# Performance work log

Measured on AMD Instinct MI355X. Metric: run time of the kernel, lower is better.

## Reference

```python
import jax, jax.numpy as jnp
import numpy as np

N_NODES = 100000
N_EDGES = 1250000
D_IN = 32
H = 64
EPS = 1e-5


def layer_norm(x, g, b):
    mu = jnp.mean(x, axis=-1, keepdims=True)
    var = jnp.mean(jnp.square(x - mu), axis=-1, keepdims=True)
    return (x - mu) * jax.lax.rsqrt(var + EPS) * g + b


def setup_inputs() -> dict:
    key = jax.random.key(0)
    ks = jax.random.split(key, 6)
    x = jax.random.normal(ks[0], (N_NODES, D_IN), dtype=jnp.float32)
    edge_index = jax.random.randint(ks[1], (2, N_EDGES), 0, N_NODES, dtype=jnp.int64)
    W1 = jax.random.normal(ks[2], (D_IN, H), dtype=jnp.float32) * (1.0 / np.sqrt(D_IN))
    b1 = jax.random.normal(ks[3], (H,), dtype=jnp.float32) * 0.01
    W2 = jax.random.normal(ks[4], (H, H), dtype=jnp.float32) * (1.0 / np.sqrt(H))
    b2 = jax.random.normal(ks[5], (H,), dtype=jnp.float32) * 0.01
    g1 = jnp.ones((H,), dtype=jnp.float32)
    beta1 = jnp.zeros((H,), dtype=jnp.float32)
    g2 = jnp.ones((H,), dtype=jnp.float32)
    beta2 = jnp.zeros((H,), dtype=jnp.float32)
    return {"x": x, "edge_index": edge_index, "W1": W1, "b1": b1, "g1": g1,
            "beta1": beta1, "W2": W2, "b2": b2, "g2": g2, "beta2": beta2}


def reference(x, edge_index, W1, b1, g1, beta1, W2, b2, g2, beta2):
    # node MLP: Linear -> LN -> ReLU, twice
    h = jax.nn.relu(layer_norm(x @ W1 + b1, g1, beta1))
    h = jax.nn.relu(layer_norm(h @ W2 + b2, g2, beta2))
    # message passing: gather source features, scatter-add to destinations
    row, col = edge_index[0], edge_index[1]
    aggr = jax.ops.segment_sum(h[col], row, num_segments=N_NODES)  # [N, H]
    return h + aggr
```

## Files before the change

kernel.cpp:

```cpp
#include <hip/hip_runtime.h>

#define N_NODES 100000
#define D_IN 32
#define H 64
#define EPS 1e-5f
#define RSTR 32
#define CAP 32
#define OV_CAP 32768

typedef float floatx2 __attribute__((ext_vector_type(2)));

__device__ __forceinline__ unsigned short f2bf(float f) {
    union { float f; unsigned int u; } c; c.f = f;
    unsigned int b = c.u + 0x7FFFu + ((c.u >> 16) & 1u);
    return (unsigned short)(b >> 16);
}
__device__ __forceinline__ float bf2f(unsigned short s) {
    union { unsigned int u; float f; } c; c.u = ((unsigned int)s) << 16;
    return c.f;
}

__global__ __launch_bounds__(256, 2) void fused_kernel(
    const float* __restrict__ x,
    const float* __restrict__ W1, const float* __restrict__ b1,
    const float* __restrict__ g1, const float* __restrict__ be1,
    const float* __restrict__ W2, const float* __restrict__ b2,
    const float* __restrict__ g2, const float* __restrict__ be2,
    unsigned short* __restrict__ hb, unsigned char* __restrict__ hb8,
    const int* __restrict__ ei, int* __restrict__ cnt, int* __restrict__ bkt,
    int* __restrict__ ovCnt, int2* __restrict__ ov,
    int E, int SB, int TOT)
{
    const int i = blockIdx.x;
    const int before = (int)((long long)i * SB / TOT);
    const int after  = (int)((long long)(i + 1) * SB / TOT);

    if (after > before) {
        int t = before * 256 + threadIdx.x;
        int e0 = t * 8;
        if (e0 >= E) return;

        int rows[8], cols[8], pos[8];
        if (e0 + 7 < E) {
            int4 r0 = *(const int4*)(ei + e0);
            int4 r1 = *(const int4*)(ei + e0 + 4);
            int4 c0 = *(const int4*)(ei + E + e0);
            int4 c1 = *(const int4*)(ei + E + e0 + 4);
            rows[0]=r0.x; rows[1]=r0.y; rows[2]=r0.z; rows[3]=r0.w;
            rows[4]=r1.x; rows[5]=r1.y; rows[6]=r1.z; rows[7]=r1.w;
            cols[0]=c0.x; cols[1]=c0.y; cols[2]=c0.z; cols[3]=c0.w;
            cols[4]=c1.x; cols[5]=c1.y; cols[6]=c1.z; cols[7]=c1.w;
        } else {
#pragma unroll
            for (int j = 0; j < 8; ++j) {
                int e = e0 + j;
                if (e < E) { rows[j] = ei[e]; cols[j] = ei[E + e]; }
                else rows[j] = -1;
            }
        }
#pragma unroll
        for (int j = 0; j < 8; ++j)
            if (rows[j] >= 0) pos[j] = atomicAdd(&cnt[rows[j]], 1);
#pragma unroll
        for (int j = 0; j < 8; ++j) {
            if (rows[j] < 0) continue;
            if (pos[j] < CAP) {
                __builtin_nontemporal_store(cols[j], &bkt[rows[j] * RSTR + pos[j]]);
            } else {
                int s = atomicAdd(ovCnt, 1);
                if (s < OV_CAP) ov[s] = make_int2(rows[j], cols[j]);
            }
        }
        return;
    }

    int gid = (i - before) * 256 + threadIdx.x;
    int node = gid < N_NODES ? gid : N_NODES - 1;

    float xr[D_IN];
    {
        const float4* xp = (const float4*)(x + (long long)node * D_IN);
#pragma unroll
        for (int i2 = 0; i2 < D_IN / 4; ++i2) {
            float4 v = xp[i2];
            xr[4*i2+0] = v.x; xr[4*i2+1] = v.y; xr[4*i2+2] = v.z; xr[4*i2+3] = v.w;
        }
    }

    float h1[H];
#pragma unroll
    for (int jb = 0; jb < H / 4; ++jb) {
        float4 b = *(const float4*)(b1 + jb * 4);
        h1[4*jb+0] = b.x; h1[4*jb+1] = b.y; h1[4*jb+2] = b.z; h1[4*jb+3] = b.w;
    }
#pragma unroll
    for (int k = 0; k < D_IN; ++k) {
        float xk = xr[k];
#pragma unroll
        for (int jb = 0; jb < H / 4; ++jb) {
            float4 w = *(const float4*)(W1 + k * H + jb * 4);
            h1[4*jb+0] += xk * w.x; h1[4*jb+1] += xk * w.y;
            h1[4*jb+2] += xk * w.z; h1[4*jb+3] += xk * w.w;
        }
    }
    {
        float s0=0,s1=0,s2=0,s3=0, q0=0,q1=0,q2=0,q3=0;
#pragma unroll
        for (int j = 0; j < H; j += 4) {
            s0 += h1[j+0]; s1 += h1[j+1]; s2 += h1[j+2]; s3 += h1[j+3];
            q0 += h1[j+0]*h1[j+0]; q1 += h1[j+1]*h1[j+1];
            q2 += h1[j+2]*h1[j+2]; q3 += h1[j+3]*h1[j+3];
        }
        float mu  = (s0+s1+s2+s3) * (1.0f / H);
        float var = (q0+q1+q2+q3) * (1.0f / H) - mu * mu;
        float rs  = rsqrtf(var + EPS);
#pragma unroll
        for (int jb = 0; jb < H / 4; ++jb) {
            float4 g = *(const float4*)(g1 + jb * 4);
            float4 be = *(const float4*)(be1 + jb * 4);
            h1[4*jb+0] = fmaxf((h1[4*jb+0]-mu)*rs*g.x + be.x, 0.0f);
            h1[4*jb+1] = fmaxf((h1[4*jb+1]-mu)*rs*g.y + be.y, 0.0f);
            h1[4*jb+2] = fmaxf((h1[4*jb+2]-mu)*rs*g.z + be.z, 0.0f);
            h1[4*jb+3] = fmaxf((h1[4*jb+3]-mu)*rs*g.w + be.w, 0.0f);
        }
    }

    float h2[H];
#pragma unroll
    for (int jb = 0; jb < H / 4; ++jb) {
        float4 b = *(const float4*)(b2 + jb * 4);
        h2[4*jb+0] = b.x; h2[4*jb+1] = b.y; h2[4*jb+2] = b.z; h2[4*jb+3] = b.w;
    }
#pragma unroll
    for (int k = 0; k < H; ++k) {
        float hk = h1[k];
#pragma unroll
        for (int jb = 0; jb < H / 4; ++jb) {
            float4 w = *(const float4*)(W2 + k * H + jb * 4);
            h2[4*jb+0] += hk * w.x; h2[4*jb+1] += hk * w.y;
            h2[4*jb+2] += hk * w.z; h2[4*jb+3] += hk * w.w;
        }
    }
    {
        float s0=0,s1=0,s2=0,s3=0, q0=0,q1=0,q2=0,q3=0;
#pragma unroll
        for (int j = 0; j < H; j += 4) {
            s0 += h2[j+0]; s1 += h2[j+1]; s2 += h2[j+2]; s3 += h2[j+3];
            q0 += h2[j+0]*h2[j+0]; q1 += h2[j+1]*h2[j+1];
            q2 += h2[j+2]*h2[j+2]; q3 += h2[j+3]*h2[j+3];
        }
        float mu  = (s0+s1+s2+s3) * (1.0f / H);
        float var = (q0+q1+q2+q3) * (1.0f / H) - mu * mu;
        float rs  = rsqrtf(var + EPS);

        unsigned short* hp = hb + (long long)node * H;
        unsigned int w8[H / 4];
#pragma unroll
        for (int jb = 0; jb < H / 4; ++jb) {
            float4 g = *(const float4*)(g2 + jb * 4);
            float4 be = *(const float4*)(be2 + jb * 4);
            float4 v;
            v.x = fmaxf((h2[4*jb+0]-mu)*rs*g.x + be.x, 0.0f);
            v.y = fmaxf((h2[4*jb+1]-mu)*rs*g.y + be.y, 0.0f);
            v.z = fmaxf((h2[4*jb+2]-mu)*rs*g.z + be.z, 0.0f);
            v.w = fmaxf((h2[4*jb+3]-mu)*rs*g.w + be.w, 0.0f);
            ushort4 u;
            u.x = f2bf(v.x); u.y = f2bf(v.y); u.z = f2bf(v.z); u.w = f2bf(v.w);
            *(ushort4*)(hp + 4*jb) = u;
            int lo = __builtin_amdgcn_cvt_pk_fp8_f32(v.x, v.y, 0, false);
            w8[jb] = (unsigned int)__builtin_amdgcn_cvt_pk_fp8_f32(v.z, v.w, lo, true);
        }
        unsigned int* hp8 = (unsigned int*)(hb8 + (long long)node * H);
#pragma unroll
        for (int q = 0; q < H / 16; ++q)
            *(uint4*)(hp8 + q * 4) = make_uint4(w8[4*q+0], w8[4*q+1], w8[4*q+2], w8[4*q+3]);
    }
}

__global__ __launch_bounds__(256, 2) void aggr_kernel(
    const int* __restrict__ cnt, const int* __restrict__ bkt,
    const unsigned short* __restrict__ hb, const unsigned char* __restrict__ hb8,
    float* __restrict__ out,
    const int* __restrict__ ovCnt, const int2* __restrict__ ov)
{
    const int t    = threadIdx.x & 63;
    const int sub  = t >> 4;
    const int c    = t & 15;
    const int wave = blockIdx.x * 4 + (threadIdx.x >> 6);
    const int node = wave * 4 + sub;

    int m = cnt[node];
    if (m > CAP) m = CAP;
    const int base = node * RSTR;
    const unsigned int* h8 = (const unsigned int*)hb8;

    float a0 = 0.f, a1 = 0.f, a2 = 0.f, a3 = 0.f;
#pragma unroll
    for (int j0 = 0; j0 < CAP; j0 += 16) {
        int cc[16];
#pragma unroll
        for (int i = 0; i < 16; ++i)
            cc[i] = bkt[base + j0 + i];
        unsigned int vv[16];
#pragma unroll
        for (int i = 0; i < 16; ++i)
            if (j0 + i < m) vv[i] = h8[(cc[i] << 4) + c];
#pragma unroll
        for (int i = 0; i < 16; ++i) {
            if (j0 + i < m) {
                floatx2 p0 = __builtin_amdgcn_cvt_pk_f32_fp8(vv[i], false);
                floatx2 p1 = __builtin_amdgcn_cvt_pk_f32_fp8(vv[i], true);
                a0 += p0.x; a1 += p0.y; a2 += p1.x; a3 += p1.y;
            }
        }
    }

    {
        uint2 sv = *(const uint2*)(hb + ((long long)node << 6) + (c << 2));
        a0 += bf2f((unsigned short)(sv.x & 0xFFFFu));
        a1 += bf2f((unsigned short)(sv.x >> 16));
        a2 += bf2f((unsigned short)(sv.y & 0xFFFFu));
        a3 += bf2f((unsigned short)(sv.y >> 16));
    }

    int nov = *ovCnt; if (nov > OV_CAP) nov = OV_CAP;
    for (int i = 0; i < nov; ++i) {
        int2 rc = ov[i];
        if (rc.x == node) {
            uint2 vv = *(const uint2*)(hb + ((long long)rc.y << 6) + (c << 2));
            a0 += bf2f((unsigned short)(vv.x & 0xFFFFu));
            a1 += bf2f((unsigned short)(vv.x >> 16));
            a2 += bf2f((unsigned short)(vv.y & 0xFFFFu));
            a3 += bf2f((unsigned short)(vv.y >> 16));
        }
    }

    *(float4*)(out + ((long long)node << 6) + (c << 2)) = make_float4(a0, a1, a2, a3);
}

extern "C" void kernel_launch(void* const* d_in, const int* in_sizes, int n_in,
                              void* d_out, int out_size, void* d_ws, size_t ws_size,
                              hipStream_t stream)
{
    const float* x   = (const float*)d_in[0];
    const int*   ei  = (const int*)d_in[1];
    const float* W1  = (const float*)d_in[2];
    const float* b1  = (const float*)d_in[3];
    const float* g1  = (const float*)d_in[4];
    const float* be1 = (const float*)d_in[5];
    const float* W2  = (const float*)d_in[6];
    const float* b2  = (const float*)d_in[7];
    const float* g2  = (const float*)d_in[8];
    const float* be2 = (const float*)d_in[9];

    float* out = (float*)d_out;

    char* ws = (char*)d_ws;
    unsigned short* hb    = (unsigned short*)ws;
    unsigned char*  hb8   = (unsigned char*)(ws + 12800000);
    int*            cnt   = (int*)(ws + 19200000);
    int*            ovCnt = (int*)(ws + 19600000);
    int2*           ov    = (int2*)(ws + 19600064);
    int*            bkt   = (int*)(ws + 19862208);

    const int E = in_sizes[1] / 2;

    hipMemsetAsync(cnt, 0, 400064, stream);

    const int SB = ((E + 7) / 8 + 255) / 256;
    const int MB = (N_NODES + 255) / 256;
    fused_kernel<<<SB + MB, 256, 0, stream>>>(
        x, W1, b1, g1, be1, W2, b2, g2, be2, hb, hb8,
        ei, cnt, bkt, ovCnt, ov, E, SB, SB + MB);

    aggr_kernel<<<N_NODES / 16, 256, 0, stream>>>(cnt, bkt, hb, hb8, out, ovCnt, ov);
}
```

Measured before the change: 206.2 us.

## Partition edge bucketing by XCD node range to localize atomics

```diff
diff --git a/kernel.cpp b/kernel.cpp
--- a/kernel.cpp
+++ b/kernel.cpp
@@ -7,8 +7,13 @@
 #define RSTR 32
 #define CAP 32
 #define OV_CAP 32768
+#define NXCD 8
+#define RNG 12500
 
 typedef float floatx2 __attribute__((ext_vector_type(2)));
+typedef int            intx4    __attribute__((ext_vector_type(4)));
+typedef unsigned int   uintx4   __attribute__((ext_vector_type(4)));
+typedef unsigned short ushortx4 __attribute__((ext_vector_type(4)));
 
 __device__ __forceinline__ unsigned short f2bf(float f) {
     union { float f; unsigned int u; } c; c.f = f;
@@ -31,21 +36,24 @@
     int* __restrict__ ovCnt, int2* __restrict__ ov,
     int E, int SB, int TOT)
 {
-    const int i = blockIdx.x;
-    const int before = (int)((long long)i * SB / TOT);
-    const int after  = (int)((long long)(i + 1) * SB / TOT);
+    const int xcd  = blockIdx.x & (NXCD - 1);
+    const int slot = blockIdx.x >> 3;
+    const int before = (int)((long long)slot * SB / TOT);
+    const int after  = (int)((long long)(slot + 1) * SB / TOT);
 
     if (after > before) {
+        const int lo = xcd * RNG;
+        const int hi = lo + RNG;
         int t = before * 256 + threadIdx.x;
         int e0 = t * 8;
         if (e0 >= E) return;
 
         int rows[8], cols[8], pos[8];
         if (e0 + 7 < E) {
-            int4 r0 = *(const int4*)(ei + e0);
-            int4 r1 = *(const int4*)(ei + e0 + 4);
-            int4 c0 = *(const int4*)(ei + E + e0);
-            int4 c1 = *(const int4*)(ei + E + e0 + 4);
+            intx4 r0 = __builtin_nontemporal_load((const intx4*)(ei + e0));
+            intx4 r1 = __builtin_nontemporal_load((const intx4*)(ei + e0 + 4));
+            intx4 c0 = __builtin_nontemporal_load((const intx4*)(ei + E + e0));
+            intx4 c1 = __builtin_nontemporal_load((const intx4*)(ei + E + e0 + 4));
             rows[0]=r0.x; rows[1]=r0.y; rows[2]=r0.z; rows[3]=r0.w;
             rows[4]=r1.x; rows[5]=r1.y; rows[6]=r1.z; rows[7]=r1.w;
             cols[0]=c0.x; cols[1]=c0.y; cols[2]=c0.z; cols[3]=c0.w;
@@ -59,13 +67,16 @@
             }
         }
 #pragma unroll
-        for (int j = 0; j < 8; ++j)
-            if (rows[j] >= 0) pos[j] = atomicAdd(&cnt[rows[j]], 1);
-#pragma unroll
         for (int j = 0; j < 8; ++j) {
-            if (rows[j] < 0) continue;
+            pos[j] = -1;
+            if (rows[j] >= lo && rows[j] < hi)
+                pos[j] = atomicAdd(&cnt[rows[j]], 1);
+        }
+#pragma unroll
+        for (int j = 0; j < 8; ++j) {
+            if (pos[j] < 0) continue;
             if (pos[j] < CAP) {
-                __builtin_nontemporal_store(cols[j], &bkt[rows[j] * RSTR + pos[j]]);
+                bkt[rows[j] * RSTR + pos[j]] = cols[j];
             } else {
                 int s = atomicAdd(ovCnt, 1);
                 if (s < OV_CAP) ov[s] = make_int2(rows[j], cols[j]);
@@ -74,7 +85,8 @@
         return;
     }
 
-    int gid = (i - before) * 256 + threadIdx.x;
+    int mlpb = (slot - before) * NXCD + xcd;
+    int gid = mlpb * 256 + threadIdx.x;
     int node = gid < N_NODES ? gid : N_NODES - 1;
 
     float xr[D_IN];
@@ -164,16 +176,19 @@
             v.y = fmaxf((h2[4*jb+1]-mu)*rs*g.y + be.y, 0.0f);
             v.z = fmaxf((h2[4*jb+2]-mu)*rs*g.z + be.z, 0.0f);
             v.w = fmaxf((h2[4*jb+3]-mu)*rs*g.w + be.w, 0.0f);
-            ushort4 u;
+            ushortx4 u;
             u.x = f2bf(v.x); u.y = f2bf(v.y); u.z = f2bf(v.z); u.w = f2bf(v.w);
-            *(ushort4*)(hp + 4*jb) = u;
-            int lo = __builtin_amdgcn_cvt_pk_fp8_f32(v.x, v.y, 0, false);
-            w8[jb] = (unsigned int)__builtin_amdgcn_cvt_pk_fp8_f32(v.z, v.w, lo, true);
+            __builtin_nontemporal_store(u, (ushortx4*)(hp + 4*jb));
+            int lo8 = __builtin_amdgcn_cvt_pk_fp8_f32(v.x, v.y, 0, false);
+            w8[jb] = (unsigned int)__builtin_amdgcn_cvt_pk_fp8_f32(v.z, v.w, lo8, true);
         }
         unsigned int* hp8 = (unsigned int*)(hb8 + (long long)node * H);
 #pragma unroll
-        for (int q = 0; q < H / 16; ++q)
-            *(uint4*)(hp8 + q * 4) = make_uint4(w8[4*q+0], w8[4*q+1], w8[4*q+2], w8[4*q+3]);
+        for (int q = 0; q < H / 16; ++q) {
+            uintx4 w;
+            w.x = w8[4*q+0]; w.y = w8[4*q+1]; w.z = w8[4*q+2]; w.w = w8[4*q+3];
+            __builtin_nontemporal_store(w, (uintx4*)(hp8 + q * 4));
+        }
     }
 }
 
@@ -265,13 +280,14 @@
 
     const int E = in_sizes[1] / 2;
 
-    hipMemsetAsync(cnt, 0, 400064, stream);
-
-    const int SB = ((E + 7) / 8 + 255) / 256;
-    const int MB = (N_NODES + 255) / 256;
-    fused_kernel<<<SB + MB, 256, 0, stream>>>(
+    (void)hipMemsetAsync(cnt, 0, 400064, stream);
+
+    const int SBX  = ((E + 7) / 8 + 255) / 256;
+    const int MBX  = (((N_NODES + 255) / 256) + NXCD - 1) / NXCD;
+    const int TOTX = SBX + MBX;
+    fused_kernel<<<NXCD * TOTX, 256, 0, stream>>>(
         x, W1, b1, g1, be1, W2, b2, g2, be2, hb, hb8,
-        ei, cnt, bkt, ovCnt, ov, E, SB, SB + MB);
+        ei, cnt, bkt, ovCnt, ov, E, SBX, TOTX);
 
     aggr_kernel<<<N_NODES / 16, 256, 0, stream>>>(cnt, bkt, hb, hb8, out, ovCnt, ov);
 }
```

Measured after the change: 214.6 us. 1.04x slower.

## Split aggregation edges across lane groups with 16-byte gathers and shuffle reduction

Applied to the files above, without the earlier changes.

```diff
diff --git a/kernel.cpp b/kernel.cpp
--- a/kernel.cpp
+++ b/kernel.cpp
@@ -185,38 +185,57 @@
 {
     const int t    = threadIdx.x & 63;
     const int sub  = t >> 4;
-    const int c    = t & 15;
+    const int l    = t & 15;
+    const int q    = l & 3;
+    const int g    = l >> 2;
     const int wave = blockIdx.x * 4 + (threadIdx.x >> 6);
     const int node = wave * 4 + sub;
 
     int m = cnt[node];
     if (m > CAP) m = CAP;
     const int base = node * RSTR;
-    const unsigned int* h8 = (const unsigned int*)hb8;
-
-    float a0 = 0.f, a1 = 0.f, a2 = 0.f, a3 = 0.f;
-#pragma unroll
-    for (int j0 = 0; j0 < CAP; j0 += 16) {
-        int cc[16];
-#pragma unroll
-        for (int i = 0; i < 16; ++i)
-            cc[i] = bkt[base + j0 + i];
-        unsigned int vv[16];
-#pragma unroll
-        for (int i = 0; i < 16; ++i)
-            if (j0 + i < m) vv[i] = h8[(cc[i] << 4) + c];
-#pragma unroll
-        for (int i = 0; i < 16; ++i) {
-            if (j0 + i < m) {
-                floatx2 p0 = __builtin_amdgcn_cvt_pk_f32_fp8(vv[i], false);
-                floatx2 p1 = __builtin_amdgcn_cvt_pk_f32_fp8(vv[i], true);
-                a0 += p0.x; a1 += p0.y; a2 += p1.x; a3 += p1.y;
+
+    int4 ea = *(const int4*)(bkt + base + g * 8);
+    int4 eb = *(const int4*)(bkt + base + g * 8 + 4);
+    int ed[8] = { ea.x, ea.y, ea.z, ea.w, eb.x, eb.y, eb.z, eb.w };
+
+    const uint4* h84 = (const uint4*)hb8;
+    const int e0 = g * 8;
+
+    float s[16];
+#pragma unroll
+    for (int j = 0; j < 16; ++j) s[j] = 0.f;
+
+    uint4 vv[8];
+#pragma unroll
+    for (int k = 0; k < 8; ++k)
+        if (e0 + k < m) vv[k] = h84[(ed[k] << 2) + q];
+
+#pragma unroll
+    for (int k = 0; k < 8; ++k) {
+        if (e0 + k < m) {
+            unsigned int w[4] = { vv[k].x, vv[k].y, vv[k].z, vv[k].w };
+#pragma unroll
+            for (int u = 0; u < 4; ++u) {
+                floatx2 p0 = __builtin_amdgcn_cvt_pk_f32_fp8(w[u], false);
+                floatx2 p1 = __builtin_amdgcn_cvt_pk_f32_fp8(w[u], true);
+                s[4*u+0] += p0.x; s[4*u+1] += p0.y;
+                s[4*u+2] += p1.x; s[4*u+3] += p1.y;
             }
         }
     }
 
-    {
-        uint2 sv = *(const uint2*)(hb + ((long long)node << 6) + (c << 2));
+#pragma unroll
+    for (int j = 0; j < 16; ++j) {
+        s[j] += __shfl_xor(s[j], 4, 64);
+        s[j] += __shfl_xor(s[j], 8, 64);
+    }
+
+    const int co = q * 16 + g * 4;
+    float a0 = s[g*4+0], a1 = s[g*4+1], a2 = s[g*4+2], a3 = s[g*4+3];
+
+    {
+        uint2 sv = *(const uint2*)(hb + ((long long)node << 6) + co);
         a0 += bf2f((unsigned short)(sv.x & 0xFFFFu));
         a1 += bf2f((unsigned short)(sv.x >> 16));
         a2 += bf2f((unsigned short)(sv.y & 0xFFFFu));
@@ -227,15 +246,15 @@
     for (int i = 0; i < nov; ++i) {
         int2 rc = ov[i];
         if (rc.x == node) {
-            uint2 vv = *(const uint2*)(hb + ((long long)rc.y << 6) + (c << 2));
-            a0 += bf2f((unsigned short)(vv.x & 0xFFFFu));
-            a1 += bf2f((unsigned short)(vv.x >> 16));
-            a2 += bf2f((unsigned short)(vv.y & 0xFFFFu));
-            a3 += bf2f((unsigned short)(vv.y >> 16));
-        }
-    }
-
-    *(float4*)(out + ((long long)node << 6) + (c << 2)) = make_float4(a0, a1, a2, a3);
+            uint2 vvо = *(const uint2*)(hb + ((long long)rc.y << 6) + co);
+            a0 += bf2f((unsigned short)(vvо.x & 0xFFFFu));
+            a1 += bf2f((unsigned short)(vvо.x >> 16));
+            a2 += bf2f((unsigned short)(vvо.y & 0xFFFFu));
+            a3 += bf2f((unsigned short)(vvо.y >> 16));
+        }
+    }
+
+    *(float4*)(out + ((long long)node << 6) + co) = make_float4(a0, a1, a2, a3);
 }
 
 extern "C" void kernel_launch(void* const* d_in, const int* in_sizes, int n_in,
@@ -265,7 +284,7 @@
 
     const int E = in_sizes[1] / 2;
 
-    hipMemsetAsync(cnt, 0, 400064, stream);
+    (void)hipMemsetAsync(cnt, 0, 400064, stream);
 
     const int SB = ((E + 7) / 8 + 255) / 256;
     const int MB = (N_NODES + 255) / 256;
```

Measured after the change: 205.9 us. About the same (-0.1%).
